# Kernel optimization log

Hardware: AMD Instinct MI355X
Metric: run time of the kernel (lower is better)

Reference implementation:

```python
import jax, jax.numpy as jnp
import numpy as np
import math

C_S = 384
C_Z = 128
N_TOK = 1024
N_ATOM = 24576
FDIM = 256
H = 4


def _layer_norm(x, g, b):
    m = jnp.mean(x, axis=-1, keepdims=True)
    v = jnp.mean((x - m) ** 2, axis=-1, keepdims=True)
    return (x - m) / jnp.sqrt(v + 1e-5) * g + b


def _forward(x_noisy, s, z, sigma, atom_to_token_idx,
             fourier_w, fourier_b, ns_w, ns_b, nz_w, nz_b,
             lns_g, lns_b, lnz_g, lnz_b, ce_w, ce_b,
             in_w, in_b, out_w, out_b,
             ffln_g, ffln_b, ff1_w, ff1_b, ff2_w, ff2_b, co_w, co_b):
    # --- DiffusionConditioning ---
    half = FDIM // 2
    freqs = jnp.exp(-math.log(1000.0) * jnp.arange(half, dtype=jnp.float32) / half)
    xf = sigma[:, None] * freqs[None, :]                      # [1, 128]
    emb = jnp.concatenate([jnp.cos(xf), jnp.sin(xf)], axis=-1)  # [1, 256]
    noise = emb @ fourier_w.T + fourier_b                     # [1, 256]
    s_cond = _layer_norm(s, lns_g, lns_b) + (noise @ ns_w.T + ns_b)   # [N_tok, c_s]
    z_cond = _layer_norm(z, lnz_g, lnz_b) + (noise @ nz_w.T + nz_b)   # [N_tok, N_tok, c_z] (unused downstream, as in torch)
    # --- atom -> token segment mean (replaces the python scatter loop) ---
    coord_feat = x_noisy @ ce_w.T + ce_b                      # [N_atom, c_s]
    n_tok = s_cond.shape[0]
    seg_sum = jax.ops.segment_sum(coord_feat, atom_to_token_idx, num_segments=n_tok)
    counts = jax.ops.segment_sum(jnp.ones((coord_feat.shape[0], 1), jnp.float32),
                                 atom_to_token_idx, num_segments=n_tok)
    token_feat = seg_sum / jnp.maximum(counts, 1.0) + s_cond  # [N_tok, c_s]
    # --- single-layer MHA (torch nn.MultiheadAttention math) ---
    qkv = token_feat @ in_w.T + in_b                          # [N_tok, 3*c_s]
    q, k, v = jnp.split(qkv, 3, axis=-1)
    D = C_S // H
    q = q.reshape(n_tok, H, D)
    k = k.reshape(n_tok, H, D)
    v = v.reshape(n_tok, H, D)
    scores = jnp.einsum('shd,thd->hst', q, k) / np.float32(np.sqrt(D))
    attn = jax.nn.softmax(scores, axis=-1)
    ao = jnp.einsum('hst,thd->shd', attn, v).reshape(n_tok, C_S)
    ao = ao @ out_w.T + out_b
    token_feat = token_feat + ao
    # --- FFN ---
    h = _layer_norm(token_feat, ffln_g, ffln_b)
    h = jax.nn.silu(h @ ff1_w.T + ff1_b) @ ff2_w.T + ff2_b
    token_feat = token_feat + h
    # --- token -> atom gather + coord head ---
    atom_feat = token_feat[atom_to_token_idx]                 # [N_atom, c_s]
    return atom_feat @ co_w.T + co_b                          # [N_atom, 3]


def setup_inputs() -> dict:
    key = jax.random.key(0)
    ks = iter(jax.random.split(key, 40))

    def lin(out_d, in_d):
        w = jax.random.normal(next(ks), (out_d, in_d), jnp.float32) / np.float32(np.sqrt(in_d))
        b = jax.random.normal(next(ks), (out_d,), jnp.float32) * 0.01
        return w, b

    fourier_w, fourier_b = lin(FDIM, FDIM)
    ns_w, ns_b = lin(C_S, FDIM)
    nz_w, nz_b = lin(C_Z, FDIM)
    ce_w, ce_b = lin(C_S, 3)
    in_w, in_b = lin(3 * C_S, C_S)
    out_w, out_b = lin(C_S, C_S)
    ff1_w, ff1_b = lin(4 * C_S, C_S)
    ff2_w, ff2_b = lin(C_S, 4 * C_S)
    co_w, co_b = lin(3, C_S)

    return {
        'x_noisy': jax.random.normal(next(ks), (N_ATOM, 3), jnp.float32),
        's': jax.random.normal(next(ks), (N_TOK, C_S), jnp.float32),
        'z': jax.random.normal(next(ks), (N_TOK, N_TOK, C_Z), jnp.float32),
        'sigma': jax.random.uniform(next(ks), (1,), jnp.float32),
        'atom_to_token_idx': jax.random.randint(next(ks), (N_ATOM,), 0, N_TOK),
        'fourier_w': fourier_w, 'fourier_b': fourier_b,
        'ns_w': ns_w, 'ns_b': ns_b, 'nz_w': nz_w, 'nz_b': nz_b,
        'lns_g': jnp.ones((C_S,), jnp.float32), 'lns_b': jnp.zeros((C_S,), jnp.float32),
        'lnz_g': jnp.ones((C_Z,), jnp.float32), 'lnz_b': jnp.zeros((C_Z,), jnp.float32),
        'ce_w': ce_w, 'ce_b': ce_b,
        'in_w': in_w, 'in_b': in_b, 'out_w': out_w, 'out_b': out_b,
        'ffln_g': jnp.ones((C_S,), jnp.float32), 'ffln_b': jnp.zeros((C_S,), jnp.float32),
        'ff1_w': ff1_w, 'ff1_b': ff1_b, 'ff2_w': ff2_w, 'ff2_b': ff2_b,
        'co_w': co_w, 'co_b': co_b,
    }


def reference(x_noisy, s, z, sigma, atom_to_token_idx,
              fourier_w, fourier_b, ns_w, ns_b, nz_w, nz_b,
              lns_g, lns_b, lnz_g, lnz_b, ce_w, ce_b,
              in_w, in_b, out_w, out_b,
              ffln_g, ffln_b, ff1_w, ff1_b, ff2_w, ff2_b, co_w, co_b):
    return _forward(x_noisy, s, z, sigma, atom_to_token_idx,
                    fourier_w, fourier_b, ns_w, ns_b, nz_w, nz_b,
                    lns_g, lns_b, lnz_g, lnz_b, ce_w, ce_b,
                    in_w, in_b, out_w, out_b,
                    ffln_g, ffln_b, ff1_w, ff1_b, ff2_w, ff2_b, co_w, co_b)
```

## Files before the change

### kernel.cpp

```cpp
#include <hip/hip_runtime.h>
#include <hip/hip_bf16.h>
#include <math.h>

#define N_TOK 1024
#define N_ATOM 24576
#define C_S 384
#define NH 4
#define HD 96

typedef __attribute__((ext_vector_type(8))) short short8;
typedef __attribute__((ext_vector_type(4))) float f32x4;

#define OFF_SEGX   0u
#define OFF_TOUT   4096u
#define OFF_NSPROJ 7424u
#define OFF_TF1    8192u
#define OFF_TF2    401408u
#define OFF_QKV    794624u
#define OFF_AOB    1384448u
#define OFF_H1B    1581056u
#define OFF_WINB   2367488u
#define OFF_WOUTB  2588672u
#define OFF_WF1B   2662400u
#define OFF_WF2B   2957312u

__device__ inline __hip_bfloat16 f2bf(float x) { return __float2bfloat16(x); }
union BFPack { short8 v; __hip_bfloat16 h[8]; };
__device__ inline short8 pack8(float4 a, float4 b)
{
    BFPack p;
    p.h[0] = f2bf(a.x); p.h[1] = f2bf(a.y); p.h[2] = f2bf(a.z); p.h[3] = f2bf(a.w);
    p.h[4] = f2bf(b.x); p.h[5] = f2bf(b.y); p.h[6] = f2bf(b.z); p.h[7] = f2bf(b.w);
    return p.v;
}

__global__ __launch_bounds__(256) void k_prep(
    const float* __restrict__ in_w, const float* __restrict__ out_w,
    const float* __restrict__ ff1_w, const float* __restrict__ ff2_w,
    __hip_bfloat16* __restrict__ winb, __hip_bfloat16* __restrict__ woutb,
    __hip_bfloat16* __restrict__ wf1b, __hip_bfloat16* __restrict__ wf2b,
    const float* __restrict__ sigma,
    const float* __restrict__ fw, const float* __restrict__ fb,
    const float* __restrict__ nsw, const float* __restrict__ nsb,
    float* __restrict__ nsproj_out, float* __restrict__ zero_base)
{
    __shared__ float emb[256];
    __shared__ float noise[256];
    int tid = threadIdx.x;
    int bid = blockIdx.x;

    if (bid == 864) {
        float sg = sigma[0];
        if (tid < 128) {
            float fr = expf(-logf(1000.f) * (float)tid / 128.f);
            float x = sg * fr;
            emb[tid]       = cosf(x);
            emb[tid + 128] = sinf(x);
        }
        __syncthreads();
        {
            const float* wr = fw + (size_t)tid * 256;
            float acc = fb[tid];
            for (int i = 0; i < 256; i++) acc += emb[i] * wr[i];
            noise[tid] = acc;
        }
        __syncthreads();
        for (int o = tid; o < 384; o += 256) {
            const float* wr = nsw + (size_t)o * 256;
            float acc = nsb[o];
            for (int i = 0; i < 256; i++) acc += noise[i] * wr[i];
            nsproj_out[o] = acc;
        }
        return;
    }
    if (bid == 0) {
        for (int i = tid; i < 7424; i += 256) zero_base[i] = 0.f;
    }
    size_t e8 = (size_t)bid * 256 + tid;
    const float* src; __hip_bfloat16* dst; size_t off;
    if (e8 < 55296)       { src = in_w;  dst = winb;  off = e8; }
    else if (e8 < 73728)  { src = out_w; dst = woutb; off = e8 - 55296; }
    else if (e8 < 147456) { src = ff1_w; dst = wf1b;  off = e8 - 73728; }
    else                  { src = ff2_w; dst = wf2b;  off = e8 - 147456; }
    float4 a = *(const float4*)(src + off * 8);
    float4 b = *(const float4*)(src + off * 8 + 4);
    *(short8*)(dst + off * 8) = pack8(a, b);
}

__global__ __launch_bounds__(256) void k_segsum(
    const float* __restrict__ x, const int* __restrict__ idx,
    float* __restrict__ segx)
{
    int a = blockIdx.x * 256 + threadIdx.x;
    if (a < N_ATOM) {
        int t = idx[a];
        atomicAdd(&segx[t * 4 + 0], x[a * 3 + 0]);
        atomicAdd(&segx[t * 4 + 1], x[a * 3 + 1]);
        atomicAdd(&segx[t * 4 + 2], x[a * 3 + 2]);
        atomicAdd(&segx[t * 4 + 3], 1.f);
    }
}

template <int MODE>
__global__ __launch_bounds__(256) void k_lngemm2(
    const float* __restrict__ X, const __hip_bfloat16* __restrict__ W,
    const float* __restrict__ bias,
    const float* __restrict__ g, const float* __restrict__ b,
    const float* __restrict__ segx, const float* __restrict__ nsproj,
    const float* __restrict__ ce_w, const float* __restrict__ ce_b,
    float* __restrict__ tf1out, __hip_bfloat16* __restrict__ OUT, int N)
{
    __shared__ __hip_bfloat16 As[64][72];
    __shared__ __hip_bfloat16 Bs[64][72];

    int tid = threadIdx.x;
    int bm = blockIdx.y * 64, bn = blockIdx.x * 64;
    int sr = tid >> 2, sc4 = tid & 3;

    const float* xrow = X + (size_t)(bm + sr) * 384;
    const float* xr = xrow + sc4 * 96;
    float s1 = 0.f, s2 = 0.f;
    #pragma unroll
    for (int i = 0; i < 24; ++i) {
        float4 v = *(const float4*)(xr + 4 * i);
        s1 += v.x + v.y + v.z + v.w;
        s2 += v.x * v.x + v.y * v.y + v.z * v.z + v.w * v.w;
    }
    s1 += __shfl_xor(s1, 1); s1 += __shfl_xor(s1, 2);
    s2 += __shfl_xor(s2, 1); s2 += __shfl_xor(s2, 2);
    float mean = s1 * (1.f / 384.f);
    float rstd = rsqrtf(s2 * (1.f / 384.f) - mean * mean + 1e-5f);

    float mx0 = 0.f, mx1 = 0.f, mx2 = 0.f;
    bool has = false;
    if (MODE == 0) {
        float cnt = segx[(bm + sr) * 4 + 3];
        has = cnt > 0.f;
        if (has) {
            float ic = 1.f / cnt;
            mx0 = segx[(bm + sr) * 4 + 0] * ic;
            mx1 = segx[(bm + sr) * 4 + 1] * ic;
            mx2 = segx[(bm + sr) * 4 + 2] * ic;
        }
    }

    int w = tid >> 6, lane = tid & 63;
    int wr = (w >> 1) * 32, wc = (w & 1) * 32;
    int fr = lane & 15, kg = lane >> 4;

    f32x4 acc[2][2] = {};
    for (int k0 = 0; k0 < 384; k0 += 64) {
        int c0 = k0 + sc4 * 16;
        short8 apack[2];
        float fv[16];
        #pragma unroll
        for (int hh = 0; hh < 2; ++hh) {
            int c = c0 + hh * 8;
            float xv[8], gv[8], bv[8], vv[8];
            *(float4*)&xv[0] = *(const float4*)(xrow + c);
            *(float4*)&xv[4] = *(const float4*)(xrow + c + 4);
            *(float4*)&gv[0] = *(const float4*)(g + c);
            *(float4*)&gv[4] = *(const float4*)(g + c + 4);
            *(float4*)&bv[0] = *(const float4*)(b + c);
            *(float4*)&bv[4] = *(const float4*)(b + c + 4);
            #pragma unroll
            for (int j = 0; j < 8; ++j)
                vv[j] = (xv[j] - mean) * rstd * gv[j] + bv[j];
            if (MODE == 0) {
                float nv[8], cb[8], ce[24];
                *(float4*)&nv[0] = *(const float4*)(nsproj + c);
                *(float4*)&nv[4] = *(const float4*)(nsproj + c + 4);
                *(float4*)&cb[0] = *(const float4*)(ce_b + c);
                *(float4*)&cb[4] = *(const float4*)(ce_b + c + 4);
                #pragma unroll
                for (int q = 0; q < 6; ++q)
                    *(float4*)&ce[q * 4] = *(const float4*)(ce_w + c * 3 + q * 4);
                #pragma unroll
                for (int j = 0; j < 8; ++j) {
                    vv[j] += nv[j];
                    if (has)
                        vv[j] += mx0 * ce[j * 3 + 0] + mx1 * ce[j * 3 + 1]
                               + mx2 * ce[j * 3 + 2] + cb[j];
                }
            }
            BFPack p;
            #pragma unroll
            for (int j = 0; j < 8; ++j) { p.h[j] = f2bf(vv[j]); fv[hh * 8 + j] = vv[j]; }
            apack[hh] = p.v;
        }
        const __hip_bfloat16* wg = W + (size_t)(bn + sr) * 384 + c0;
        short8 bb0 = *(const short8*)(wg + 0);
        short8 bb1 = *(const short8*)(wg + 8);
        __syncthreads();
        *(short8*)&As[sr][sc4 * 16 + 0] = apack[0];
        *(short8*)&As[sr][sc4 * 16 + 8] = apack[1];
        *(short8*)&Bs[sr][sc4 * 16 + 0] = bb0;
        *(short8*)&Bs[sr][sc4 * 16 + 8] = bb1;
        __syncthreads();
        if (MODE == 0 && blockIdx.x == 0) {
            float* dst = tf1out + (size_t)(bm + sr) * 384 + c0;
            *(float4*)(dst + 0)  = *(float4*)&fv[0];
            *(float4*)(dst + 4)  = *(float4*)&fv[4];
            *(float4*)(dst + 8)  = *(float4*)&fv[8];
            *(float4*)(dst + 12) = *(float4*)&fv[12];
        }

        short8 af[2][2], bf[2][2];
        #pragma unroll
        for (int i = 0; i < 2; ++i)
            #pragma unroll
            for (int kh = 0; kh < 2; ++kh) {
                af[i][kh] = *(const short8*)&As[wr + i * 16 + fr][kh * 32 + kg * 8];
                bf[i][kh] = *(const short8*)&Bs[wc + i * 16 + fr][kh * 32 + kg * 8];
            }
        #pragma unroll
        for (int kh = 0; kh < 2; ++kh)
            #pragma unroll
            for (int i = 0; i < 2; ++i)
                #pragma unroll
                for (int j = 0; j < 2; ++j)
                    acc[i][j] = __builtin_amdgcn_mfma_f32_16x16x32_bf16(
                        af[i][kh], bf[j][kh], acc[i][j], 0, 0, 0);
    }

    #pragma unroll
    for (int i = 0; i < 2; ++i)
        #pragma unroll
        for (int j = 0; j < 2; ++j) {
            int n = bn + wc + j * 16 + fr;
            float bsv = bias[n];
            #pragma unroll
            for (int r = 0; r < 4; ++r) {
                int m = bm + wr + i * 16 + kg * 4 + r;
                float v = acc[i][j][r] + bsv;
                if (MODE == 1) v = v / (1.f + __expf(-v));
                OUT[(size_t)m * N + n] = f2bf(v);
            }
        }
}

__global__ __launch_bounds__(256) void k_gemm_res(
    const __hip_bfloat16* __restrict__ A, const __hip_bfloat16* __restrict__ W,
    const float* __restrict__ bias, const float* __restrict__ res,
    float* __restrict__ C, int M, int N, int K)
{
    __shared__ __hip_bfloat16 As[64][72];
    __shared__ __hip_bfloat16 Bs[64][72];

    int tid = threadIdx.x;
    int bm = blockIdx.y * 64, bn = blockIdx.x * 64;
    int w = tid >> 6, lane = tid & 63;
    int wr = (w >> 1) * 32, wc = (w & 1) * 32;
    int fr = lane & 15, kg = lane >> 4;
    int sr = tid >> 2, sc = (tid & 3) << 4;

    f32x4 acc[2][2] = {};
    for (int k0 = 0; k0 < K; k0 += 64) {
        const __hip_bfloat16* ag = A + (size_t)(bm + sr) * K + k0 + sc;
        const __hip_bfloat16* wg = W + (size_t)(bn + sr) * K + k0 + sc;
        short8 a0 = *(const short8*)(ag + 0);
        short8 a1 = *(const short8*)(ag + 8);
        short8 b0 = *(const short8*)(wg + 0);
        short8 b1 = *(const short8*)(wg + 8);
        __syncthreads();
        *(short8*)&As[sr][sc + 0] = a0;
        *(short8*)&As[sr][sc + 8] = a1;
        *(short8*)&Bs[sr][sc + 0] = b0;
        *(short8*)&Bs[sr][sc + 8] = b1;
        __syncthreads();

        short8 af[2][2], bf[2][2];
        #pragma unroll
        for (int i = 0; i < 2; ++i)
            #pragma unroll
            for (int kh = 0; kh < 2; ++kh) {
                af[i][kh] = *(const short8*)&As[wr + i * 16 + fr][kh * 32 + kg * 8];
                bf[i][kh] = *(const short8*)&Bs[wc + i * 16 + fr][kh * 32 + kg * 8];
            }
        #pragma unroll
        for (int kh = 0; kh < 2; ++kh)
            #pragma unroll
            for (int i = 0; i < 2; ++i)
                #pragma unroll
                for (int j = 0; j < 2; ++j)
                    acc[i][j] = __builtin_amdgcn_mfma_f32_16x16x32_bf16(
                        af[i][kh], bf[j][kh], acc[i][j], 0, 0, 0);
    }

    #pragma unroll
    for (int i = 0; i < 2; ++i)
        #pragma unroll
        for (int j = 0; j < 2; ++j) {
            int n = bn + wc + j * 16 + fr;
            float bv = bias[n];
            #pragma unroll
            for (int r = 0; r < 4; ++r) {
                int m = bm + wr + i * 16 + kg * 4 + r;
                C[(size_t)m * N + n] = acc[i][j][r] + bv + res[(size_t)m * N + n];
            }
        }
}

__global__ __launch_bounds__(256) void k_gemm_tout(
    const __hip_bfloat16* __restrict__ A, const __hip_bfloat16* __restrict__ W,
    const float* __restrict__ bias, const float* __restrict__ res,
    const float* __restrict__ co_w, float* __restrict__ tout, int K)
{
    __shared__ __hip_bfloat16 As[64][72];
    __shared__ __hip_bfloat16 Bs[64][72];

    int tid = threadIdx.x;
    int bm = blockIdx.y * 64, bn = blockIdx.x * 64;
    int w = tid >> 6, lane = tid & 63;
    int wr = (w >> 1) * 32, wc = (w & 1) * 32;
    int fr = lane & 15, kg = lane >> 4;
    int sr = tid >> 2, sc = (tid & 3) << 4;

    f32x4 acc[2][2] = {};
    for (int k0 = 0; k0 < K; k0 += 64) {
        const __hip_bfloat16* ag = A + (size_t)(bm + sr) * K + k0 + sc;
        const __hip_bfloat16* wg = W + (size_t)(bn + sr) * K + k0 + sc;
        short8 a0 = *(const short8*)(ag + 0);
        short8 a1 = *(const short8*)(ag + 8);
        short8 b0 = *(const short8*)(wg + 0);
        short8 b1 = *(const short8*)(wg + 8);
        __syncthreads();
        *(short8*)&As[sr][sc + 0] = a0;
        *(short8*)&As[sr][sc + 8] = a1;
        *(short8*)&Bs[sr][sc + 0] = b0;
        *(short8*)&Bs[sr][sc + 8] = b1;
        __syncthreads();

        short8 af[2][2], bf[2][2];
        #pragma unroll
        for (int i = 0; i < 2; ++i)
            #pragma unroll
            for (int kh = 0; kh < 2; ++kh) {
                af[i][kh] = *(const short8*)&As[wr + i * 16 + fr][kh * 32 + kg * 8];
                bf[i][kh] = *(const short8*)&Bs[wc + i * 16 + fr][kh * 32 + kg * 8];
            }
        #pragma unroll
        for (int kh = 0; kh < 2; ++kh)
            #pragma unroll
            for (int i = 0; i < 2; ++i)
                #pragma unroll
                for (int j = 0; j < 2; ++j)
                    acc[i][j] = __builtin_amdgcn_mfma_f32_16x16x32_bf16(
                        af[i][kh], bf[j][kh], acc[i][j], 0, 0, 0);
    }

    float part[2][4][3] = {};
    #pragma unroll
    for (int j = 0; j < 2; ++j) {
        int n = bn + wc + j * 16 + fr;
        float bv = bias[n];
        float c0 = co_w[n], c1 = co_w[384 + n], c2 = co_w[768 + n];
        #pragma unroll
        for (int i = 0; i < 2; ++i)
            #pragma unroll
            for (int r = 0; r < 4; ++r) {
                int m = bm + wr + i * 16 + kg * 4 + r;
                float v = acc[i][j][r] + bv + res[(size_t)m * 384 + n];
                part[i][r][0] += v * c0;
                part[i][r][1] += v * c1;
                part[i][r][2] += v * c2;
            }
    }
    #pragma unroll
    for (int off = 1; off < 16; off <<= 1)
        #pragma unroll
        for (int i = 0; i < 2; ++i)
            #pragma unroll
            for (int r = 0; r < 4; ++r)
                #pragma unroll
                for (int jj = 0; jj < 3; ++jj)
                    part[i][r][jj] += __shfl_xor(part[i][r][jj], off);
    if (fr == 0)
        #pragma unroll
        for (int i = 0; i < 2; ++i)
            #pragma unroll
            for (int r = 0; r < 4; ++r) {
                int m = bm + wr + i * 16 + kg * 4 + r;
                #pragma unroll
                for (int jj = 0; jj < 3; ++jj)
                    atomicAdd(&tout[m * 3 + jj], part[i][r][jj]);
            }
}

#define QB 32
#define TB 64

__global__ __launch_bounds__(256) void k_attn(
    const __hip_bfloat16* __restrict__ qkv, __hip_bfloat16* __restrict__ ao)
{
    __shared__ __hip_bfloat16 Ks[TB][104];
    __shared__ __hip_bfloat16 Vt[96][72];
    __shared__ __hip_bfloat16 Ps[QB][72];
    __shared__ float wmax[QB][4];
    __shared__ float wsum[QB][4];

    int tid = threadIdx.x;
    int w = tid >> 6, l = tid & 63;
    int fr = l & 15, kg = l >> 4;
    int row0 = blockIdx.x * QB;
    int h = blockIdx.y;
    const float scale = 0.1020620726f;

    short8 qf[2][3];
    #pragma unroll
    for (int qs = 0; qs < 2; ++qs)
        #pragma unroll
        for (int dg = 0; dg < 3; ++dg)
            qf[qs][dg] = *(const short8*)(qkv
                + (size_t)(row0 + qs * 16 + fr) * 1152 + h * 96 + dg * 32 + kg * 8);

    float m[2][4], lsum[2][4];
    #pragma unroll
    for (int qs = 0; qs < 2; ++qs)
        #pragma unroll
        for (int r = 0; r < 4; ++r) { m[qs][r] = -1e30f; lsum[qs][r] = 0.f; }

    const int myqs = w >> 1;
    const int d0 = (w & 1) * 48;
    f32x4 acc_o[3] = {};

    int st_t = tid >> 2, st_c = (tid & 3) * 24;
    int vt_t = tid & 63, vt_d = (tid >> 6) * 24;

    for (int tile = 0; tile < N_TOK / TB; ++tile) {
        int t0 = tile * TB;
        __syncthreads();
        {
            const __hip_bfloat16* src =
                qkv + (size_t)(t0 + st_t) * 1152 + 384 + h * 96 + st_c;
            short8 k0 = *(const short8*)(src);
            short8 k1 = *(const short8*)(src + 8);
            short8 k2 = *(const short8*)(src + 16);
            *(short8*)&Ks[st_t][st_c + 0]  = k0;
            *(short8*)&Ks[st_t][st_c + 8]  = k1;
            *(short8*)&Ks[st_t][st_c + 16] = k2;
        }
        {
            const __hip_bfloat16* src =
                qkv + (size_t)(t0 + vt_t) * 1152 + 768 + h * 96 + vt_d;
            BFPack p0, p1, p2;
            p0.v = *(const short8*)(src);
            p1.v = *(const short8*)(src + 8);
            p2.v = *(const short8*)(src + 16);
            #pragma unroll
            for (int j = 0; j < 8; ++j) {
                Vt[vt_d + j][vt_t]      = p0.h[j];
                Vt[vt_d + 8 + j][vt_t]  = p1.h[j];
                Vt[vt_d + 16 + j][vt_t] = p2.h[j];
            }
        }
        __syncthreads();

        f32x4 s[2] = {};
        #pragma unroll
        for (int dg = 0; dg < 3; ++dg) {
            short8 kf = *(const short8*)&Ks[w * 16 + fr][dg * 32 + kg * 8];
            s[0] = __builtin_amdgcn_mfma_f32_16x16x32_bf16(qf[0][dg], kf, s[0], 0, 0, 0);
            s[1] = __builtin_amdgcn_mfma_f32_16x16x32_bf16(qf[1][dg], kf, s[1], 0, 0, 0);
        }

        #pragma unroll
        for (int qs = 0; qs < 2; ++qs) {
            float rmax[4];
            #pragma unroll
            for (int r = 0; r < 4; ++r) rmax[r] = s[qs][r] * scale;
            #pragma unroll
            for (int off = 1; off < 16; off <<= 1)
                #pragma unroll
                for (int r = 0; r < 4; ++r)
                    rmax[r] = fmaxf(rmax[r], __shfl_xor(rmax[r], off));
            if (fr == 0)
                #pragma unroll
                for (int r = 0; r < 4; ++r)
                    wmax[qs * 16 + kg * 4 + r][w] = rmax[r];
        }
        __syncthreads();

        float sc_my[4];
        #pragma unroll
        for (int qs = 0; qs < 2; ++qs) {
            float psum[4];
            #pragma unroll
            for (int r = 0; r < 4; ++r) {
                int row = qs * 16 + kg * 4 + r;
                float4 wm = *(const float4*)&wmax[row][0];
                float gm = fmaxf(fmaxf(wm.x, wm.y), fmaxf(wm.z, wm.w));
                float mnew = fmaxf(m[qs][r], gm);
                float scr = __expf(m[qs][r] - mnew);
                float p = __expf(s[qs][r] * scale - mnew);
                m[qs][r] = mnew;
                lsum[qs][r] *= scr;
                if (qs == myqs) sc_my[r] = scr;
                Ps[row][w * 16 + fr] = f2bf(p);
                psum[r] = p;
            }
            #pragma unroll
            for (int off = 1; off < 16; off <<= 1)
                #pragma unroll
                for (int r = 0; r < 4; ++r)
                    psum[r] += __shfl_xor(psum[r], off);
            if (fr == 0)
                #pragma unroll
                for (int r = 0; r < 4; ++r)
                    wsum[qs * 16 + kg * 4 + r][w] = psum[r];
        }
        __syncthreads();

        #pragma unroll
        for (int qs = 0; qs < 2; ++qs)
            #pragma unroll
            for (int r = 0; r < 4; ++r) {
                float4 wsv = *(const float4*)&wsum[qs * 16 + kg * 4 + r][0];
                lsum[qs][r] += wsv.x + wsv.y + wsv.z + wsv.w;
            }

        #pragma unroll
        for (int ds = 0; ds < 3; ++ds)
            #pragma unroll
            for (int r = 0; r < 4; ++r)
                acc_o[ds][r] *= sc_my[r];
        #pragma unroll
        for (int kk = 0; kk < 2; ++kk) {
            short8 pf = *(const short8*)&Ps[myqs * 16 + fr][kk * 32 + kg * 8];
            #pragma unroll
            for (int ds = 0; ds < 3; ++ds) {
                short8 vf = *(const short8*)&Vt[d0 + ds * 16 + fr][kk * 32 + kg * 8];
                acc_o[ds] = __builtin_amdgcn_mfma_f32_16x16x32_bf16(pf, vf, acc_o[ds], 0, 0, 0);
            }
        }
    }

    #pragma unroll
    for (int r = 0; r < 4; ++r) {
        float inv = 1.f / lsum[myqs][r];
        int q = row0 + myqs * 16 + kg * 4 + r;
        #pragma unroll
        for (int ds = 0; ds < 3; ++ds) {
            int d = h * 96 + d0 + ds * 16 + fr;
            ao[(size_t)q * C_S + d] = f2bf(acc_o[ds][r] * inv);
        }
    }
}

__global__ __launch_bounds__(256) void k_gather(
    const float* __restrict__ tout, const int* __restrict__ idx,
    const float* __restrict__ co_b, float* __restrict__ out)
{
    int a = blockIdx.x * 256 + threadIdx.x;
    if (a < N_ATOM) {
        int t = idx[a];
        out[a * 3 + 0] = tout[t * 3 + 0] + co_b[0];
        out[a * 3 + 1] = tout[t * 3 + 1] + co_b[1];
        out[a * 3 + 2] = tout[t * 3 + 2] + co_b[2];
    }
}

extern "C" void kernel_launch(void* const* d_in, const int* in_sizes, int n_in,
                              void* d_out, int out_size, void* d_ws, size_t ws_size,
                              hipStream_t stream)
{
    const float* x_noisy   = (const float*)d_in[0];
    const float* s         = (const float*)d_in[1];
    const float* sigma     = (const float*)d_in[3];
    const int*   a2t       = (const int*)d_in[4];
    const float* fourier_w = (const float*)d_in[5];
    const float* fourier_b = (const float*)d_in[6];
    const float* ns_w      = (const float*)d_in[7];
    const float* ns_b      = (const float*)d_in[8];
    const float* lns_g     = (const float*)d_in[11];
    const float* lns_b     = (const float*)d_in[12];
    const float* ce_w      = (const float*)d_in[15];
    const float* ce_b      = (const float*)d_in[16];
    const float* in_w      = (const float*)d_in[17];
    const float* in_b      = (const float*)d_in[18];
    const float* out_w     = (const float*)d_in[19];
    const float* out_b     = (const float*)d_in[20];
    const float* ffln_g    = (const float*)d_in[21];
    const float* ffln_b    = (const float*)d_in[22];
    const float* ff1_w     = (const float*)d_in[23];
    const float* ff1_b     = (const float*)d_in[24];
    const float* ff2_w     = (const float*)d_in[25];
    const float* ff2_b     = (const float*)d_in[26];
    const float* co_w      = (const float*)d_in[27];
    const float* co_b      = (const float*)d_in[28];

    float* ws  = (float*)d_ws;
    float* out = (float*)d_out;
    __hip_bfloat16* qkvb  = (__hip_bfloat16*)(ws + OFF_QKV);
    __hip_bfloat16* aob   = (__hip_bfloat16*)(ws + OFF_AOB);
    __hip_bfloat16* h1b   = (__hip_bfloat16*)(ws + OFF_H1B);
    __hip_bfloat16* winb  = (__hip_bfloat16*)(ws + OFF_WINB);
    __hip_bfloat16* woutb = (__hip_bfloat16*)(ws + OFF_WOUTB);
    __hip_bfloat16* wf1b  = (__hip_bfloat16*)(ws + OFF_WF1B);
    __hip_bfloat16* wf2b  = (__hip_bfloat16*)(ws + OFF_WF2B);

    hipLaunchKernelGGL(k_prep, dim3(865), dim3(256), 0, stream,
                       in_w, out_w, ff1_w, ff2_w, winb, woutb, wf1b, wf2b,
                       sigma, fourier_w, fourier_b, ns_w, ns_b,
                       ws + OFF_NSPROJ, ws);
    hipLaunchKernelGGL(k_segsum, dim3(96), dim3(256), 0, stream,
                       x_noisy, a2t, ws + OFF_SEGX);
    hipLaunchKernelGGL((k_lngemm2<0>), dim3(18, 16), dim3(256), 0, stream,
                       s, winb, in_b, lns_g, lns_b,
                       ws + OFF_SEGX, ws + OFF_NSPROJ, ce_w, ce_b,
                       ws + OFF_TF1, qkvb, 1152);
    hipLaunchKernelGGL(k_attn, dim3(N_TOK / QB, NH), dim3(256), 0, stream,
                       qkvb, aob);
    hipLaunchKernelGGL(k_gemm_res, dim3(6, 16), dim3(256), 0, stream,
                       aob, woutb, out_b, ws + OFF_TF1, ws + OFF_TF2,
                       1024, 384, 384);
    hipLaunchKernelGGL((k_lngemm2<1>), dim3(24, 16), dim3(256), 0, stream,
                       ws + OFF_TF2, wf1b, ff1_b, ffln_g, ffln_b,
                       nullptr, nullptr, nullptr, nullptr,
                       nullptr, h1b, 1536);
    hipLaunchKernelGGL(k_gemm_tout, dim3(6, 16), dim3(256), 0, stream,
                       h1b, wf2b, ff2_b, ws + OFF_TF2, co_w,
                       ws + OFF_TOUT, 1536);
    hipLaunchKernelGGL(k_gather, dim3(96), dim3(256), 0, stream,
                       ws + OFF_TOUT, a2t, co_b, out);
}
```

Baseline: 168.6 us.

## Split token-feature LN into own kernel and fuse FFN LN stats into out-proj epilogue

The fused LN+QKV GEMM is split into a per-token kernel that computes the conditioned token features once, writing fp32 and bf16 copies, followed by a plain bf16 GEMM. This removes the LayerNorm and coordinate-embedding math that each of the 18 column blocks used to recompute. The output-projection GEMM now accumulates per-row sum and sum-of-squares with atomics, so the FFN LayerNorm GEMM no longer re-reads each row to get its statistics. The cost is one extra launch, an extra bf16 buffer write and read, and atomic contention on the row statistics.

```diff
diff --git a/kernel.cpp b/kernel.cpp
--- a/kernel.cpp
+++ b/kernel.cpp
@@ -13,16 +13,18 @@
 
 #define OFF_SEGX   0u
 #define OFF_TOUT   4096u
-#define OFF_NSPROJ 7424u
-#define OFF_TF1    8192u
-#define OFF_TF2    401408u
-#define OFF_QKV    794624u
-#define OFF_AOB    1384448u
-#define OFF_H1B    1581056u
-#define OFF_WINB   2367488u
-#define OFF_WOUTB  2588672u
-#define OFF_WF1B   2662400u
-#define OFF_WF2B   2957312u
+#define OFF_RSTAT  7424u
+#define OFF_NSPROJ 9472u
+#define OFF_TF1    9984u
+#define OFF_TF2    403200u
+#define OFF_TF1B   796416u
+#define OFF_QKV    993024u
+#define OFF_AOB    1582848u
+#define OFF_H1B    1779456u
+#define OFF_WINB   2565888u
+#define OFF_WOUTB  2787072u
+#define OFF_WF1B   2860800u
+#define OFF_WF2B   3155712u
 
 __device__ inline __hip_bfloat16 f2bf(float x) { return __float2bfloat16(x); }
 union BFPack { short8 v; __hip_bfloat16 h[8]; };
@@ -74,7 +76,7 @@
         return;
     }
     if (bid == 0) {
-        for (int i = tid; i < 7424; i += 256) zero_base[i] = 0.f;
+        for (int i = tid; i < 9472; i += 256) zero_base[i] = 0.f;
     }
     size_t e8 = (size_t)bid * 256 + tid;
     const float* src; __hip_bfloat16* dst; size_t off;
@@ -101,148 +103,61 @@
     }
 }
 
-template <int MODE>
-__global__ __launch_bounds__(256) void k_lngemm2(
-    const float* __restrict__ X, const __hip_bfloat16* __restrict__ W,
-    const float* __restrict__ bias,
+__device__ inline float blockReduceSum128(float v, volatile float* sm)
+{
+    #pragma unroll
+    for (int off = 32; off > 0; off >>= 1) v += __shfl_down(v, off);
+    if ((threadIdx.x & 63) == 0) sm[threadIdx.x >> 6] = v;
+    __syncthreads();
+    float r = sm[0] + sm[1];
+    __syncthreads();
+    return r;
+}
+
+__global__ __launch_bounds__(128) void k_tokenfeat(
+    const float* __restrict__ s, const float* __restrict__ segx,
+    const float* __restrict__ nsproj,
     const float* __restrict__ g, const float* __restrict__ b,
-    const float* __restrict__ segx, const float* __restrict__ nsproj,
     const float* __restrict__ ce_w, const float* __restrict__ ce_b,
-    float* __restrict__ tf1out, __hip_bfloat16* __restrict__ OUT, int N)
-{
-    __shared__ __hip_bfloat16 As[64][72];
-    __shared__ __hip_bfloat16 Bs[64][72];
-
-    int tid = threadIdx.x;
-    int bm = blockIdx.y * 64, bn = blockIdx.x * 64;
-    int sr = tid >> 2, sc4 = tid & 3;
-
-    const float* xrow = X + (size_t)(bm + sr) * 384;
-    const float* xr = xrow + sc4 * 96;
-    float s1 = 0.f, s2 = 0.f;
-    #pragma unroll
-    for (int i = 0; i < 24; ++i) {
-        float4 v = *(const float4*)(xr + 4 * i);
-        s1 += v.x + v.y + v.z + v.w;
-        s2 += v.x * v.x + v.y * v.y + v.z * v.z + v.w * v.w;
-    }
-    s1 += __shfl_xor(s1, 1); s1 += __shfl_xor(s1, 2);
-    s2 += __shfl_xor(s2, 1); s2 += __shfl_xor(s2, 2);
-    float mean = s1 * (1.f / 384.f);
-    float rstd = rsqrtf(s2 * (1.f / 384.f) - mean * mean + 1e-5f);
-
+    float* __restrict__ tf, __hip_bfloat16* __restrict__ tfb)
+{
+    __shared__ float sm[2];
+    int t = blockIdx.x, tid = threadIdx.x;
+    const float* sr = s + (size_t)t * C_S;
+    float x0 = sr[tid], x1 = sr[tid + 128], x2 = sr[tid + 256];
+    float total = blockReduceSum128(x0 + x1 + x2, sm);
+    float mean = total * (1.f / 384.f);
+    float d0 = x0 - mean, d1 = x1 - mean, d2 = x2 - mean;
+    float vtot = blockReduceSum128(d0 * d0 + d1 * d1 + d2 * d2, sm);
+    float inv = rsqrtf(vtot * (1.f / 384.f) + 1e-5f);
+    float cnt = segx[t * 4 + 3];
     float mx0 = 0.f, mx1 = 0.f, mx2 = 0.f;
-    bool has = false;
-    if (MODE == 0) {
-        float cnt = segx[(bm + sr) * 4 + 3];
-        has = cnt > 0.f;
-        if (has) {
-            float ic = 1.f / cnt;
-            mx0 = segx[(bm + sr) * 4 + 0] * ic;
-            mx1 = segx[(bm + sr) * 4 + 1] * ic;
-            mx2 = segx[(bm + sr) * 4 + 2] * ic;
-        }
-    }
-
-    int w = tid >> 6, lane = tid & 63;
-    int wr = (w >> 1) * 32, wc = (w & 1) * 32;
-    int fr = lane & 15, kg = lane >> 4;
-
-    f32x4 acc[2][2] = {};
-    for (int k0 = 0; k0 < 384; k0 += 64) {
-        int c0 = k0 + sc4 * 16;
-        short8 apack[2];
-        float fv[16];
-        #pragma unroll
-        for (int hh = 0; hh < 2; ++hh) {
-            int c = c0 + hh * 8;
-            float xv[8], gv[8], bv[8], vv[8];
-            *(float4*)&xv[0] = *(const float4*)(xrow + c);
-            *(float4*)&xv[4] = *(const float4*)(xrow + c + 4);
-            *(float4*)&gv[0] = *(const float4*)(g + c);
-            *(float4*)&gv[4] = *(const float4*)(g + c + 4);
-            *(float4*)&bv[0] = *(const float4*)(b + c);
-            *(float4*)&bv[4] = *(const float4*)(b + c + 4);
-            #pragma unroll
-            for (int j = 0; j < 8; ++j)
-                vv[j] = (xv[j] - mean) * rstd * gv[j] + bv[j];
-            if (MODE == 0) {
-                float nv[8], cb[8], ce[24];
-                *(float4*)&nv[0] = *(const float4*)(nsproj + c);
-                *(float4*)&nv[4] = *(const float4*)(nsproj + c + 4);
-                *(float4*)&cb[0] = *(const float4*)(ce_b + c);
-                *(float4*)&cb[4] = *(const float4*)(ce_b + c + 4);
-                #pragma unroll
-                for (int q = 0; q < 6; ++q)
-                    *(float4*)&ce[q * 4] = *(const float4*)(ce_w + c * 3 + q * 4);
-                #pragma unroll
-                for (int j = 0; j < 8; ++j) {
-                    vv[j] += nv[j];
-                    if (has)
-                        vv[j] += mx0 * ce[j * 3 + 0] + mx1 * ce[j * 3 + 1]
-                               + mx2 * ce[j * 3 + 2] + cb[j];
-                }
-            }
-            BFPack p;
-            #pragma unroll
-            for (int j = 0; j < 8; ++j) { p.h[j] = f2bf(vv[j]); fv[hh * 8 + j] = vv[j]; }
-            apack[hh] = p.v;
-        }
-        const __hip_bfloat16* wg = W + (size_t)(bn + sr) * 384 + c0;
-        short8 bb0 = *(const short8*)(wg + 0);
-        short8 bb1 = *(const short8*)(wg + 8);
-        __syncthreads();
-        *(short8*)&As[sr][sc4 * 16 + 0] = apack[0];
-        *(short8*)&As[sr][sc4 * 16 + 8] = apack[1];
-        *(short8*)&Bs[sr][sc4 * 16 + 0] = bb0;
-        *(short8*)&Bs[sr][sc4 * 16 + 8] = bb1;
-        __syncthreads();
-        if (MODE == 0 && blockIdx.x == 0) {
-            float* dst = tf1out + (size_t)(bm + sr) * 384 + c0;
-            *(float4*)(dst + 0)  = *(float4*)&fv[0];
-            *(float4*)(dst + 4)  = *(float4*)&fv[4];
-            *(float4*)(dst + 8)  = *(float4*)&fv[8];
-            *(float4*)(dst + 12) = *(float4*)&fv[12];
-        }
-
-        short8 af[2][2], bf[2][2];
-        #pragma unroll
-        for (int i = 0; i < 2; ++i)
-            #pragma unroll
-            for (int kh = 0; kh < 2; ++kh) {
-                af[i][kh] = *(const short8*)&As[wr + i * 16 + fr][kh * 32 + kg * 8];
-                bf[i][kh] = *(const short8*)&Bs[wc + i * 16 + fr][kh * 32 + kg * 8];
-            }
-        #pragma unroll
-        for (int kh = 0; kh < 2; ++kh)
-            #pragma unroll
-            for (int i = 0; i < 2; ++i)
-                #pragma unroll
-                for (int j = 0; j < 2; ++j)
-                    acc[i][j] = __builtin_amdgcn_mfma_f32_16x16x32_bf16(
-                        af[i][kh], bf[j][kh], acc[i][j], 0, 0, 0);
-    }
-
-    #pragma unroll
-    for (int i = 0; i < 2; ++i)
-        #pragma unroll
-        for (int j = 0; j < 2; ++j) {
-            int n = bn + wc + j * 16 + fr;
-            float bsv = bias[n];
-            #pragma unroll
-            for (int r = 0; r < 4; ++r) {
-                int m = bm + wr + i * 16 + kg * 4 + r;
-                float v = acc[i][j][r] + bsv;
-                if (MODE == 1) v = v / (1.f + __expf(-v));
-                OUT[(size_t)m * N + n] = f2bf(v);
-            }
-        }
-}
-
-__global__ __launch_bounds__(256) void k_gemm_res(
+    int has = cnt > 0.f;
+    if (has) {
+        float ic = 1.f / cnt;
+        mx0 = segx[t * 4 + 0] * ic;
+        mx1 = segx[t * 4 + 1] * ic;
+        mx2 = segx[t * 4 + 2] * ic;
+    }
+    float xs[3] = {d0, d1, d2};
+    #pragma unroll
+    for (int l = 0; l < 3; l++) {
+        int c = tid + l * 128;
+        float ln = xs[l] * inv * g[c] + b[c];
+        float coord = 0.f;
+        if (has)
+            coord = mx0 * ce_w[c * 3 + 0] + mx1 * ce_w[c * 3 + 1]
+                  + mx2 * ce_w[c * 3 + 2] + ce_b[c];
+        float v = ln + nsproj[c] + coord;
+        tf[(size_t)t * C_S + c] = v;
+        tfb[(size_t)t * C_S + c] = f2bf(v);
+    }
+}
+
+__global__ __launch_bounds__(256) void k_gemm_obf(
     const __hip_bfloat16* __restrict__ A, const __hip_bfloat16* __restrict__ W,
-    const float* __restrict__ bias, const float* __restrict__ res,
-    float* __restrict__ C, int M, int N, int K)
+    const float* __restrict__ bias, __hip_bfloat16* __restrict__ C,
+    int N, int K)
 {
     __shared__ __hip_bfloat16 As[64][72];
     __shared__ __hip_bfloat16 Bs[64][72];
@@ -296,7 +211,178 @@
             #pragma unroll
             for (int r = 0; r < 4; ++r) {
                 int m = bm + wr + i * 16 + kg * 4 + r;
-                C[(size_t)m * N + n] = acc[i][j][r] + bv + res[(size_t)m * N + n];
+                C[(size_t)m * N + n] = f2bf(acc[i][j][r] + bv);
+            }
+        }
+}
+
+__global__ __launch_bounds__(256) void k_gemm_res_stats(
+    const __hip_bfloat16* __restrict__ A, const __hip_bfloat16* __restrict__ W,
+    const float* __restrict__ bias, const float* __restrict__ res,
+    float* __restrict__ C, float* __restrict__ rstat, int N, int K)
+{
+    __shared__ __hip_bfloat16 As[64][72];
+    __shared__ __hip_bfloat16 Bs[64][72];
+
+    int tid = threadIdx.x;
+    int bm = blockIdx.y * 64, bn = blockIdx.x * 64;
+    int w = tid >> 6, lane = tid & 63;
+    int wr = (w >> 1) * 32, wc = (w & 1) * 32;
+    int fr = lane & 15, kg = lane >> 4;
+    int sr = tid >> 2, sc = (tid & 3) << 4;
+
+    f32x4 acc[2][2] = {};
+    for (int k0 = 0; k0 < K; k0 += 64) {
+        const __hip_bfloat16* ag = A + (size_t)(bm + sr) * K + k0 + sc;
+        const __hip_bfloat16* wg = W + (size_t)(bn + sr) * K + k0 + sc;
+        short8 a0 = *(const short8*)(ag + 0);
+        short8 a1 = *(const short8*)(ag + 8);
+        short8 b0 = *(const short8*)(wg + 0);
+        short8 b1 = *(const short8*)(wg + 8);
+        __syncthreads();
+        *(short8*)&As[sr][sc + 0] = a0;
+        *(short8*)&As[sr][sc + 8] = a1;
+        *(short8*)&Bs[sr][sc + 0] = b0;
+        *(short8*)&Bs[sr][sc + 8] = b1;
+        __syncthreads();
+
+        short8 af[2][2], bf[2][2];
+        #pragma unroll
+        for (int i = 0; i < 2; ++i)
+            #pragma unroll
+            for (int kh = 0; kh < 2; ++kh) {
+                af[i][kh] = *(const short8*)&As[wr + i * 16 + fr][kh * 32 + kg * 8];
+                bf[i][kh] = *(const short8*)&Bs[wc + i * 16 + fr][kh * 32 + kg * 8];
+            }
+        #pragma unroll
+        for (int kh = 0; kh < 2; ++kh)
+            #pragma unroll
+            for (int i = 0; i < 2; ++i)
+                #pragma unroll
+                for (int j = 0; j < 2; ++j)
+                    acc[i][j] = __builtin_amdgcn_mfma_f32_16x16x32_bf16(
+                        af[i][kh], bf[j][kh], acc[i][j], 0, 0, 0);
+    }
+
+    float st0[2][4] = {}, st1[2][4] = {};
+    #pragma unroll
+    for (int i = 0; i < 2; ++i)
+        #pragma unroll
+        for (int j = 0; j < 2; ++j) {
+            int n = bn + wc + j * 16 + fr;
+            float bv = bias[n];
+            #pragma unroll
+            for (int r = 0; r < 4; ++r) {
+                int m = bm + wr + i * 16 + kg * 4 + r;
+                float v = acc[i][j][r] + bv + res[(size_t)m * N + n];
+                C[(size_t)m * N + n] = v;
+                st0[i][r] += v;
+                st1[i][r] += v * v;
+            }
+        }
+    #pragma unroll
+    for (int off = 1; off < 16; off <<= 1)
+        #pragma unroll
+        for (int i = 0; i < 2; ++i)
+            #pragma unroll
+            for (int r = 0; r < 4; ++r) {
+                st0[i][r] += __shfl_xor(st0[i][r], off);
+                st1[i][r] += __shfl_xor(st1[i][r], off);
+            }
+    if (fr == 0)
+        #pragma unroll
+        for (int i = 0; i < 2; ++i)
+            #pragma unroll
+            for (int r = 0; r < 4; ++r) {
+                int m = bm + wr + i * 16 + kg * 4 + r;
+                atomicAdd(&rstat[m * 2 + 0], st0[i][r]);
+                atomicAdd(&rstat[m * 2 + 1], st1[i][r]);
+            }
+}
+
+__global__ __launch_bounds__(256) void k_lnff1(
+    const float* __restrict__ X, const __hip_bfloat16* __restrict__ W,
+    const float* __restrict__ bias,
+    const float* __restrict__ g, const float* __restrict__ b,
+    const float* __restrict__ rstat, __hip_bfloat16* __restrict__ OUT)
+{
+    __shared__ __hip_bfloat16 As[64][72];
+    __shared__ __hip_bfloat16 Bs[64][72];
+
+    int tid = threadIdx.x;
+    int bm = blockIdx.y * 64, bn = blockIdx.x * 64;
+    int sr = tid >> 2, sc4 = tid & 3;
+
+    const float* xrow = X + (size_t)(bm + sr) * 384;
+    float s1 = rstat[(bm + sr) * 2 + 0];
+    float s2 = rstat[(bm + sr) * 2 + 1];
+    float mean = s1 * (1.f / 384.f);
+    float rstd = rsqrtf(s2 * (1.f / 384.f) - mean * mean + 1e-5f);
+
+    int w = tid >> 6, lane = tid & 63;
+    int wr = (w >> 1) * 32, wc = (w & 1) * 32;
+    int fr = lane & 15, kg = lane >> 4;
+
+    f32x4 acc[2][2] = {};
+    for (int k0 = 0; k0 < 384; k0 += 64) {
+        int c0 = k0 + sc4 * 16;
+        short8 apack[2];
+        #pragma unroll
+        for (int hh = 0; hh < 2; ++hh) {
+            int c = c0 + hh * 8;
+            float xv[8], gv[8], bv[8];
+            *(float4*)&xv[0] = *(const float4*)(xrow + c);
+            *(float4*)&xv[4] = *(const float4*)(xrow + c + 4);
+            *(float4*)&gv[0] = *(const float4*)(g + c);
+            *(float4*)&gv[4] = *(const float4*)(g + c + 4);
+            *(float4*)&bv[0] = *(const float4*)(b + c);
+            *(float4*)&bv[4] = *(const float4*)(b + c + 4);
+            BFPack p;
+            #pragma unroll
+            for (int j = 0; j < 8; ++j)
+                p.h[j] = f2bf((xv[j] - mean) * rstd * gv[j] + bv[j]);
+            apack[hh] = p.v;
+        }
+        const __hip_bfloat16* wg = W + (size_t)(bn + sr) * 384 + c0;
+        short8 bb0 = *(const short8*)(wg + 0);
+        short8 bb1 = *(const short8*)(wg + 8);
+        __syncthreads();
+        *(short8*)&As[sr][sc4 * 16 + 0] = apack[0];
+        *(short8*)&As[sr][sc4 * 16 + 8] = apack[1];
+        *(short8*)&Bs[sr][sc4 * 16 + 0] = bb0;
+        *(short8*)&Bs[sr][sc4 * 16 + 8] = bb1;
+        __syncthreads();
+
+        short8 af[2][2], bf[2][2];
+        #pragma unroll
+        for (int i = 0; i < 2; ++i)
+            #pragma unroll
+            for (int kh = 0; kh < 2; ++kh) {
+                af[i][kh] = *(const short8*)&As[wr + i * 16 + fr][kh * 32 + kg * 8];
+                bf[i][kh] = *(const short8*)&Bs[wc + i * 16 + fr][kh * 32 + kg * 8];
+            }
+        #pragma unroll
+        for (int kh = 0; kh < 2; ++kh)
+            #pragma unroll
+            for (int i = 0; i < 2; ++i)
+                #pragma unroll
+                for (int j = 0; j < 2; ++j)
+                    acc[i][j] = __builtin_amdgcn_mfma_f32_16x16x32_bf16(
+                        af[i][kh], bf[j][kh], acc[i][j], 0, 0, 0);
+    }
+
+    #pragma unroll
+    for (int i = 0; i < 2; ++i)
+        #pragma unroll
+        for (int j = 0; j < 2; ++j) {
+            int n = bn + wc + j * 16 + fr;
+            float bsv = bias[n];
+            #pragma unroll
+            for (int r = 0; r < 4; ++r) {
+                int m = bm + wr + i * 16 + kg * 4 + r;
+                float v = acc[i][j][r] + bsv;
+                v = v / (1.f + __expf(-v));
+                OUT[(size_t)m * 1536 + n] = f2bf(v);
             }
         }
 }
@@ -591,6 +677,7 @@
 
     float* ws  = (float*)d_ws;
     float* out = (float*)d_out;
+    __hip_bfloat16* tf1b  = (__hip_bfloat16*)(ws + OFF_TF1B);
     __hip_bfloat16* qkvb  = (__hip_bfloat16*)(ws + OFF_QKV);
     __hip_bfloat16* aob   = (__hip_bfloat16*)(ws + OFF_AOB);
     __hip_bfloat16* h1b   = (__hip_bfloat16*)(ws + OFF_H1B);
@@ -605,19 +692,19 @@
                        ws + OFF_NSPROJ, ws);
     hipLaunchKernelGGL(k_segsum, dim3(96), dim3(256), 0, stream,
                        x_noisy, a2t, ws + OFF_SEGX);
-    hipLaunchKernelGGL((k_lngemm2<0>), dim3(18, 16), dim3(256), 0, stream,
-                       s, winb, in_b, lns_g, lns_b,
-                       ws + OFF_SEGX, ws + OFF_NSPROJ, ce_w, ce_b,
-                       ws + OFF_TF1, qkvb, 1152);
+    hipLaunchKernelGGL(k_tokenfeat, dim3(N_TOK), dim3(128), 0, stream,
+                       s, ws + OFF_SEGX, ws + OFF_NSPROJ, lns_g, lns_b,
+                       ce_w, ce_b, ws + OFF_TF1, tf1b);
+    hipLaunchKernelGGL(k_gemm_obf, dim3(18, 16), dim3(256), 0, stream,
+                       tf1b, winb, in_b, qkvb, 1152, 384);
     hipLaunchKernelGGL(k_attn, dim3(N_TOK / QB, NH), dim3(256), 0, stream,
                        qkvb, aob);
-    hipLaunchKernelGGL(k_gemm_res, dim3(6, 16), dim3(256), 0, stream,
+    hipLaunchKernelGGL(k_gemm_res_stats, dim3(6, 16), dim3(256), 0, stream,
                        aob, woutb, out_b, ws + OFF_TF1, ws + OFF_TF2,
-                       1024, 384, 384);
-    hipLaunchKernelGGL((k_lngemm2<1>), dim3(24, 16), dim3(256), 0, stream,
+                       ws + OFF_RSTAT, 384, 384);
+    hipLaunchKernelGGL(k_lnff1, dim3(24, 16), dim3(256), 0, stream,
                        ws + OFF_TF2, wf1b, ff1_b, ffln_g, ffln_b,
-                       nullptr, nullptr, nullptr, nullptr,
-                       nullptr, h1b, 1536);
+                       ws + OFF_RSTAT, h1b);
     hipLaunchKernelGGL(k_gemm_tout, dim3(6, 16), dim3(256), 0, stream,
                        h1b, wf2b, ff2_b, ws + OFF_TF2, co_w,
                        ws + OFF_TOUT, 1536);
```

After: 140.2 us. 16.9% less time.
